# Kernel tuning notes

Hardware: AMD Instinct MI355X
Metric: run time of the kernel (lower is better)

The kernel has to match this reference:

```python
import jax, jax.numpy as jnp
import numpy as np

N = 1024
IN_CH = 128
EDGE_CH = 32
OUT_CH = 128


def setup_inputs() -> dict:
    key = jax.random.key(0)
    ks = jax.random.split(key, 8)
    return {
        "node_mat": jax.random.normal(ks[0], (N, IN_CH), dtype=jnp.float32),
        "adj": jax.random.uniform(ks[1], (N, N), dtype=jnp.float32),
        "edge_adj": jax.random.uniform(ks[2], (EDGE_CH, N, N), dtype=jnp.float32),
        "node_weight": jax.random.normal(ks[3], (IN_CH, OUT_CH), dtype=jnp.float32) * 0.05,
        "edge_lay_1": jax.random.normal(ks[4], (EDGE_CH, OUT_CH - 1), dtype=jnp.float32) * 0.05,
        "edge_lay_2": jax.random.normal(ks[5], (OUT_CH - 1, OUT_CH), dtype=jnp.float32) * 0.05,
        "root": jax.random.normal(ks[6], (IN_CH, OUT_CH), dtype=jnp.float32) * 0.05,
        "bias": jax.random.normal(ks[7], (OUT_CH,), dtype=jnp.float32) * 0.05,
    }


def reference(node_mat, adj, edge_adj, node_weight, edge_lay_1, edge_lay_2, root, bias):
    # node message passing: adj-weighted sum of transformed node features  [N, out]
    sum_filter_node_msgs = adj @ (node_mat @ node_weight)
    # edge MLP: 2-layer with ReLU, applied over the edge-channel axis
    # edge_adj: [E, N, N]; edge_lay_1: [E, out-1] -> h1: [out-1, N, N]
    h1 = jnp.maximum(jnp.einsum('enm,eb->bnm', edge_adj, edge_lay_1), 0.0)
    # h1: [out-1, N, N]; edge_lay_2: [out-1, out] -> h2: [out, N, N]
    h2 = jnp.einsum('bnm,bo->onm', h1, edge_lay_2)
    # adjacency-weighted compression: e_compress[n, o] = sum_m h2[o, n, m] * adj[n, m]
    e_compress = jnp.einsum('onm,nm->no', h2, adj)
    root_info = node_mat @ root
    return sum_filter_node_msgs + e_compress + root_info + bias
```

## Files before the change

kernel.cpp:

```cpp
#include <hip/hip_runtime.h>
#include <hip/hip_bf16.h>

#define NN 1024
#define IN_CH 128
#define EDGE_CH 32
#define OUT_CH 128

typedef __attribute__((ext_vector_type(8))) short bf16x8;
typedef __attribute__((ext_vector_type(4))) float f32x4;

static __device__ __forceinline__ short f2bf(float f) {
    union { float f; unsigned u; } v; v.f = f;
    unsigned r = v.u + 0x7FFFu + ((v.u >> 16) & 1u);
    return (short)(r >> 16);
}

static __device__ __forceinline__ void async_copy16(const float* gptr, float* lptr) {
    __builtin_amdgcn_global_load_lds(
        (const __attribute__((address_space(1))) void*)gptr,
        (__attribute__((address_space(3))) void*)lptr,
        16, 0, 0);
}

__global__ void node_gemm_kernel(const float* __restrict__ node_mat,
                                 const float* __restrict__ node_weight,
                                 const float* __restrict__ root,
                                 float* __restrict__ PF,
                                 float* __restrict__ R) {
    int tid = threadIdx.x;
    int wave = tid >> 6, lane = tid & 63, quad = lane >> 4, col = lane & 15;
    int m0 = blockIdx.x * 16;

    f32x4 accP[2] = {{0.f,0.f,0.f,0.f},{0.f,0.f,0.f,0.f}};
    f32x4 accR[2] = {{0.f,0.f,0.f,0.f},{0.f,0.f,0.f,0.f}};

#pragma unroll
    for (int ks = 0; ks < 4; ++ks) {
        bf16x8 a;
#pragma unroll
        for (int j = 0; j < 8; ++j)
            a[j] = f2bf(node_mat[(m0 + col) * IN_CH + ks * 32 + quad * 8 + j]);
#pragma unroll
        for (int t = 0; t < 2; ++t) {
            int ob = (wave * 2 + t) * 16;
            bf16x8 bw, br;
#pragma unroll
            for (int j = 0; j < 8; ++j) {
                int k = ks * 32 + quad * 8 + j;
                bw[j] = f2bf(node_weight[k * OUT_CH + ob + col]);
                br[j] = f2bf(root[k * OUT_CH + ob + col]);
            }
            accP[t] = __builtin_amdgcn_mfma_f32_16x16x32_bf16(a, bw, accP[t], 0, 0, 0);
            accR[t] = __builtin_amdgcn_mfma_f32_16x16x32_bf16(a, br, accR[t], 0, 0, 0);
        }
    }
#pragma unroll
    for (int t = 0; t < 2; ++t)
#pragma unroll
        for (int r = 0; r < 4; ++r) {
            int m = m0 + quad * 4 + r;
            int o = (wave * 2 + t) * 16 + col;
            PF[(size_t)m * OUT_CH + o] = accP[t][r];
            R[(size_t)m * OUT_CH + o]  = accR[t][r];
        }
}

__global__ void __launch_bounds__(256)
fused_kernel(const float* __restrict__ edge_adj,
             const float* __restrict__ adj,
             const float* __restrict__ L1,
             const float* __restrict__ L2,
             const float* __restrict__ PF,
             const float* __restrict__ R,
             const float* __restrict__ bias,
             float* __restrict__ out) {
    __shared__ float ea_lds[2][8 * 260];
    __shared__ float adj_lds[NN];
    __shared__ float gs[OUT_CH];
    __shared__ float part[2][OUT_CH];

    int n = blockIdx.x;
    int tid = threadIdx.x;
    int wave = tid >> 6, lane = tid & 63, quad = lane >> 4, col = lane & 15;

    bf16x8 a_frag[2];
#pragma unroll
    for (int t = 0; t < 2; ++t) {
        int b = wave * 32 + t * 16 + col;
#pragma unroll
        for (int j = 0; j < 8; ++j) {
            int e = quad * 8 + j;
            a_frag[t][j] = (b < OUT_CH - 1) ? f2bf(L1[e * (OUT_CH - 1) + b]) : (short)0;
        }
    }
    float g_acc[2][4] = {{0.f,0.f,0.f,0.f},{0.f,0.f,0.f,0.f}};

    const float* gsrc = edge_adj + (size_t)n * NN;
    size_t eoff0 = ((size_t)(2 * wave + 0) * 4 + (lane >> 4)) * (size_t)(NN * NN)
                 + (size_t)((lane & 15) * 4);
    size_t eoff1 = ((size_t)(2 * wave + 1) * 4 + (lane >> 4)) * (size_t)(NN * NN)
                 + (size_t)((lane & 15) * 4);
    float* dst0 = &ea_lds[0][(2 * wave + 0) * 260];
    float* dst1 = &ea_lds[0][(2 * wave + 1) * 260];
    float* dst0b = &ea_lds[1][(2 * wave + 0) * 260];
    float* dst1b = &ea_lds[1][(2 * wave + 1) * 260];

    async_copy16(gsrc + eoff0, dst0);
    async_copy16(gsrc + eoff1, dst1);
    async_copy16(adj + (size_t)n * NN + wave * 256 + lane * 4, &adj_lds[wave * 256]);
    async_copy16(gsrc + eoff0 + 64, dst0b);
    async_copy16(gsrc + eoff1 + 64, dst1b);

    for (int c = 0; c < 16; ++c) {
        if (c < 15) __builtin_amdgcn_s_waitcnt(0xF72);
        else        __builtin_amdgcn_s_waitcnt(0xF70);
        __syncthreads();

        const float* eb = ea_lds[c & 1];
#pragma unroll
        for (int s = 0; s < 4; ++s) {
            float adjv = adj_lds[c * 64 + s * 16 + col];
            bf16x8 bf;
#pragma unroll
            for (int j = 0; j < 8; ++j) {
                int e = quad * 8 + j;
                bf[j] = f2bf(eb[(e >> 2) * 260 + (e & 3) * 64 + s * 16 + col]);
            }
#pragma unroll
            for (int t = 0; t < 2; ++t) {
                f32x4 d = __builtin_amdgcn_mfma_f32_16x16x32_bf16(
                    a_frag[t], bf, (f32x4){0.f, 0.f, 0.f, 0.f}, 0, 0, 0);
#pragma unroll
                for (int r = 0; r < 4; ++r)
                    g_acc[t][r] += fmaxf(d[r], 0.0f) * adjv;
            }
        }
        __syncthreads();

        if (c < 14) {
            int nc = c + 2;
            float* d0 = &ea_lds[nc & 1][(2 * wave + 0) * 260];
            float* d1 = &ea_lds[nc & 1][(2 * wave + 1) * 260];
            async_copy16(gsrc + eoff0 + nc * 64, d0);
            async_copy16(gsrc + eoff1 + nc * 64, d1);
        }
    }

#pragma unroll
    for (int t = 0; t < 2; ++t)
#pragma unroll
        for (int r = 0; r < 4; ++r) {
            float v = g_acc[t][r];
            v += __shfl_xor(v, 1);
            v += __shfl_xor(v, 2);
            v += __shfl_xor(v, 4);
            v += __shfl_xor(v, 8);
            if (col == 0) gs[wave * 32 + t * 16 + quad * 4 + r] = v;
        }
    __syncthreads();

    int o = tid & 127;
    int hf = tid >> 7;
    float acc = 0.f;
    int blo = hf * 64, bhi = hf ? (OUT_CH - 1) : 64;
#pragma unroll 8
    for (int b = blo; b < bhi; ++b)
        acc += gs[b] * L2[b * OUT_CH + o];

    float a0 = 0.f, a1 = 0.f, a2 = 0.f, a3 = 0.f;
    const float* pf = PF + (size_t)(hf * 512) * OUT_CH + o;
    const float* aw = &adj_lds[hf * 512];
    for (int mm = 0; mm < 512; mm += 4) {
        a0 += aw[mm + 0] * pf[(size_t)(mm + 0) * OUT_CH];
        a1 += aw[mm + 1] * pf[(size_t)(mm + 1) * OUT_CH];
        a2 += aw[mm + 2] * pf[(size_t)(mm + 2) * OUT_CH];
        a3 += aw[mm + 3] * pf[(size_t)(mm + 3) * OUT_CH];
    }
    acc += (a0 + a1) + (a2 + a3);
    part[hf][o] = acc;
    __syncthreads();
    if (tid < 128)
        out[(size_t)n * OUT_CH + tid] =
            part[0][tid] + part[1][tid] + R[(size_t)n * OUT_CH + tid] + bias[tid];
}

extern "C" void kernel_launch(void* const* d_in, const int* in_sizes, int n_in,
                              void* d_out, int out_size, void* d_ws, size_t ws_size,
                              hipStream_t stream) {
    const float* node_mat    = (const float*)d_in[0];
    const float* adj         = (const float*)d_in[1];
    const float* edge_adj    = (const float*)d_in[2];
    const float* node_weight = (const float*)d_in[3];
    const float* edge_lay_1  = (const float*)d_in[4];
    const float* edge_lay_2  = (const float*)d_in[5];
    const float* root        = (const float*)d_in[6];
    const float* bias        = (const float*)d_in[7];
    float* out = (float*)d_out;

    float* PF = (float*)d_ws;
    float* R  = PF + NN * OUT_CH;

    node_gemm_kernel<<<64, 256, 0, stream>>>(node_mat, node_weight, root, PF, R);
    fused_kernel<<<NN, 256, 0, stream>>>(edge_adj, adj, edge_lay_1, edge_lay_2,
                                         PF, R, bias, out);
}
```

Baseline: 262.4 us.

## Rework edge MLP wave split, triple-buffer edge tiles, pack bf16 loads

Each wave now covers 64 hidden channels over half the spatial columns instead of 32 channels over all columns. Each bf16 B fragment is therefore reused across four MFMAs, and the LDS read and convert work per wave is halved. Edge tiles move from double to triple buffering, which lets one of the two block barriers per chunk go. The bf16 pack uses a cheaper round-half-up conversion, and the launch bounds request four blocks per CU. The cost is an extra cross-wave reduction through LDS and more accumulator registers.

Result: slower. 585.4 us (+123.1%).

```diff
diff --git a/kernel.cpp b/kernel.cpp
--- a/kernel.cpp
+++ b/kernel.cpp
@@ -5,14 +5,22 @@
 #define IN_CH 128
 #define EDGE_CH 32
 #define OUT_CH 128
+#define UDW 260
 
 typedef __attribute__((ext_vector_type(8))) short bf16x8;
 typedef __attribute__((ext_vector_type(4))) float f32x4;
+typedef __attribute__((ext_vector_type(4))) unsigned u32x4;
 
 static __device__ __forceinline__ short f2bf(float f) {
     union { float f; unsigned u; } v; v.f = f;
     unsigned r = v.u + 0x7FFFu + ((v.u >> 16) & 1u);
     return (short)(r >> 16);
+}
+
+static __device__ __forceinline__ unsigned pack_bf2(float lo, float hi) {
+    unsigned ulo = __float_as_uint(lo) + 0x8000u;
+    unsigned uhi = __float_as_uint(hi) + 0x8000u;
+    return (uhi & 0xFFFF0000u) | (ulo >> 16);
 }
 
 static __device__ __forceinline__ void async_copy16(const float* gptr, float* lptr) {
@@ -65,7 +73,7 @@
         }
 }
 
-__global__ void __launch_bounds__(256)
+__global__ void __launch_bounds__(256, 4)
 fused_kernel(const float* __restrict__ edge_adj,
              const float* __restrict__ adj,
              const float* __restrict__ L1,
@@ -74,89 +82,94 @@
              const float* __restrict__ R,
              const float* __restrict__ bias,
              float* __restrict__ out) {
-    __shared__ float ea_lds[2][8 * 260];
+    __shared__ float ea_lds[3][8 * UDW];
     __shared__ float adj_lds[NN];
+    __shared__ float gred[4][64];
     __shared__ float gs[OUT_CH];
     __shared__ float part[2][OUT_CH];
 
     int n = blockIdx.x;
     int tid = threadIdx.x;
     int wave = tid >> 6, lane = tid & 63, quad = lane >> 4, col = lane & 15;
-
-    bf16x8 a_frag[2];
-#pragma unroll
-    for (int t = 0; t < 2; ++t) {
-        int b = wave * 32 + t * 16 + col;
+    int h  = wave & 1;
+    int bh = wave >> 1;
+
+    bf16x8 a_frag[4];
+#pragma unroll
+    for (int bt = 0; bt < 4; ++bt) {
+        int b = bh * 64 + bt * 16 + col;
 #pragma unroll
         for (int j = 0; j < 8; ++j) {
             int e = quad * 8 + j;
-            a_frag[t][j] = (b < OUT_CH - 1) ? f2bf(L1[e * (OUT_CH - 1) + b]) : (short)0;
-        }
-    }
-    float g_acc[2][4] = {{0.f,0.f,0.f,0.f},{0.f,0.f,0.f,0.f}};
-
-    const float* gsrc = edge_adj + (size_t)n * NN;
-    size_t eoff0 = ((size_t)(2 * wave + 0) * 4 + (lane >> 4)) * (size_t)(NN * NN)
-                 + (size_t)((lane & 15) * 4);
-    size_t eoff1 = ((size_t)(2 * wave + 1) * 4 + (lane >> 4)) * (size_t)(NN * NN)
-                 + (size_t)((lane & 15) * 4);
-    float* dst0 = &ea_lds[0][(2 * wave + 0) * 260];
-    float* dst1 = &ea_lds[0][(2 * wave + 1) * 260];
-    float* dst0b = &ea_lds[1][(2 * wave + 0) * 260];
-    float* dst1b = &ea_lds[1][(2 * wave + 1) * 260];
-
-    async_copy16(gsrc + eoff0, dst0);
-    async_copy16(gsrc + eoff1, dst1);
+            a_frag[bt][j] = (b < OUT_CH - 1) ? f2bf(L1[e * (OUT_CH - 1) + b]) : (short)0;
+        }
+    }
+    float g_acc[4][4];
+#pragma unroll
+    for (int bt = 0; bt < 4; ++bt)
+#pragma unroll
+        for (int r = 0; r < 4; ++r) g_acc[bt][r] = 0.f;
+
+    const float* g0 = edge_adj + (size_t)(8 * wave + (lane >> 4)) * (size_t)(NN * NN)
+                    + (size_t)n * NN + (lane & 15) * 4;
+    const float* g1 = g0 + (size_t)4 * NN * NN;
+
+    async_copy16(g0, &ea_lds[0][(2 * wave + 0) * UDW]);
+    async_copy16(g1, &ea_lds[0][(2 * wave + 1) * UDW]);
     async_copy16(adj + (size_t)n * NN + wave * 256 + lane * 4, &adj_lds[wave * 256]);
-    async_copy16(gsrc + eoff0 + 64, dst0b);
-    async_copy16(gsrc + eoff1 + 64, dst1b);
-
+    async_copy16(g0 + 64, &ea_lds[1][(2 * wave + 0) * UDW]);
+    async_copy16(g1 + 64, &ea_lds[1][(2 * wave + 1) * UDW]);
+
+#pragma unroll
     for (int c = 0; c < 16; ++c) {
         if (c < 15) __builtin_amdgcn_s_waitcnt(0xF72);
         else        __builtin_amdgcn_s_waitcnt(0xF70);
-        __syncthreads();
-
-        const float* eb = ea_lds[c & 1];
-#pragma unroll
-        for (int s = 0; s < 4; ++s) {
+        __builtin_amdgcn_s_barrier();
+
+        const float* b0 = &ea_lds[c % 3][(2 * quad + 0) * UDW + col];
+        const float* b1 = b0 + UDW;
+#pragma unroll
+        for (int ss = 0; ss < 2; ++ss) {
+            int s = h * 2 + ss;
             float adjv = adj_lds[c * 64 + s * 16 + col];
-            bf16x8 bf;
-#pragma unroll
-            for (int j = 0; j < 8; ++j) {
-                int e = quad * 8 + j;
-                bf[j] = f2bf(eb[(e >> 2) * 260 + (e & 3) * 64 + s * 16 + col]);
+            u32x4 pk;
+            pk[0] = pack_bf2(b0[s * 16],       b0[s * 16 + 64]);
+            pk[1] = pack_bf2(b0[s * 16 + 128], b0[s * 16 + 192]);
+            pk[2] = pack_bf2(b1[s * 16],       b1[s * 16 + 64]);
+            pk[3] = pack_bf2(b1[s * 16 + 128], b1[s * 16 + 192]);
+            bf16x8 bf = __builtin_bit_cast(bf16x8, pk);
+#pragma unroll
+            for (int bt = 0; bt < 4; ++bt) {
+                f32x4 d = __builtin_amdgcn_mfma_f32_16x16x32_bf16(
+                    a_frag[bt], bf, (f32x4){0.f, 0.f, 0.f, 0.f}, 0, 0, 0);
+#pragma unroll
+                for (int r = 0; r < 4; ++r)
+                    g_acc[bt][r] += fmaxf(d[r], 0.0f) * adjv;
             }
-#pragma unroll
-            for (int t = 0; t < 2; ++t) {
-                f32x4 d = __builtin_amdgcn_mfma_f32_16x16x32_bf16(
-                    a_frag[t], bf, (f32x4){0.f, 0.f, 0.f, 0.f}, 0, 0, 0);
-#pragma unroll
-                for (int r = 0; r < 4; ++r)
-                    g_acc[t][r] += fmaxf(d[r], 0.0f) * adjv;
-            }
-        }
-        __syncthreads();
+        }
 
         if (c < 14) {
             int nc = c + 2;
-            float* d0 = &ea_lds[nc & 1][(2 * wave + 0) * 260];
-            float* d1 = &ea_lds[nc & 1][(2 * wave + 1) * 260];
-            async_copy16(gsrc + eoff0 + nc * 64, d0);
-            async_copy16(gsrc + eoff1 + nc * 64, d1);
-        }
-    }
-
-#pragma unroll
-    for (int t = 0; t < 2; ++t)
+            async_copy16(g0 + nc * 64, &ea_lds[nc % 3][(2 * wave + 0) * UDW]);
+            async_copy16(g1 + nc * 64, &ea_lds[nc % 3][(2 * wave + 1) * UDW]);
+        }
+    }
+
+#pragma unroll
+    for (int bt = 0; bt < 4; ++bt)
 #pragma unroll
         for (int r = 0; r < 4; ++r) {
-            float v = g_acc[t][r];
+            float v = g_acc[bt][r];
             v += __shfl_xor(v, 1);
             v += __shfl_xor(v, 2);
             v += __shfl_xor(v, 4);
             v += __shfl_xor(v, 8);
-            if (col == 0) gs[wave * 32 + t * 16 + quad * 4 + r] = v;
-        }
+            if (col == 0) gred[wave][bt * 16 + quad * 4 + r] = v;
+        }
+    __syncthreads();
+    if (tid < OUT_CH)
+        gs[tid] = (tid < 64) ? (gred[0][tid] + gred[1][tid])
+                             : (gred[2][tid - 64] + gred[3][tid - 64]);
     __syncthreads();
 
     int o = tid & 127;
```
